# Kernel tuning notes

Hardware: AMD Instinct MI355X
Metric: run time of the kernel (lower is better)

Reference implementation:

```python
import jax, jax.numpy as jnp
import numpy as np

N = 100000          # n_nodes
E = 1600000         # n_edges (avg degree 16)
IN = 256            # in_dim
OUT = 16            # out_dim
SLOPE = 0.2         # leaky_relu negative slope
DROP = 0.5          # dropout rate


def _xavier(key, shape):
    fan_in, fan_out = shape
    std = (2.0 / (fan_in + fan_out)) ** 0.5
    return std * jax.random.normal(key, shape, jnp.float32)


def setup_inputs() -> dict:
    key = jax.random.key(0)
    ks = jax.random.split(key, 10)
    x = jax.random.normal(ks[0], (N, IN), jnp.float32)
    row = jax.random.randint(ks[1], (E,), 0, N, jnp.int32)
    col = jax.random.randint(ks[2], (E,), 0, N, jnp.int32)
    edge_w = jax.random.uniform(ks[3], (E,), jnp.float32)
    W1 = _xavier(ks[4], (IN, IN // 2)); b1 = jnp.zeros((IN // 2,), jnp.float32)
    W2 = _xavier(ks[5], (IN // 2, IN // 4)); b2 = jnp.zeros((IN // 4,), jnp.float32)
    W3 = _xavier(ks[6], (IN // 4, IN // 8)); b3 = jnp.zeros((IN // 8,), jnp.float32)
    W4 = _xavier(ks[7], (IN // 8, OUT)); b4 = jnp.zeros((OUT,), jnp.float32)
    # dropout mask (training-mode dropout made deterministic; pre-scaled by 1/(1-p))
    drop_mask = (jax.random.uniform(ks[8], (N, IN // 2)) > DROP).astype(jnp.float32) / (1.0 - DROP)
    return dict(x=x, row=row, col=col, edge_w=edge_w,
                W1=W1, b1=b1, W2=W2, b2=b2, W3=W3, b3=b3, W4=W4, b4=b4,
                drop_mask=drop_mask)


def reference(x, row, col, edge_w, W1, b1, W2, b2, W3, b3, W4, b4, drop_mask):
    def spmm(h):
        # out[i] = sum over edges (i <- j): w_ij * h[j]   (sparse adj @ h)
        return jax.ops.segment_sum(edge_w[:, None] * h[col], row, num_segments=N)

    lrelu = lambda v: jax.nn.leaky_relu(v, SLOPE)

    h = spmm(x @ W1) + b1          # gc1: [N, IN/2]
    h = lrelu(h) * drop_mask       # leaky_relu + dropout
    h = spmm(h @ W2) + b2          # gc2: [N, IN/4]
    h = lrelu(h)
    h = lrelu(h @ W3 + b3)         # clf hidden: [N, IN/8]
    return h @ W4 + b4             # logits: [N, OUT]
```

## Files before the change

kernel.cpp:

```cpp
#include <hip/hip_runtime.h>
#include <hip/hip_bf16.h>

#define N_NODES 100000
#define N_EDGES 1600000
#define SLOPE_ 0.2f
#define NBK 196
#define BCAP 9216
#define NCB 25
#define KEYS (512 * NCB)
#define BINBLK 256

typedef __attribute__((ext_vector_type(8))) short bf16x8;
typedef __attribute__((ext_vector_type(4))) float f32x4;

__device__ __forceinline__ short f2bf(float f) {
    __hip_bfloat16 h = __float2bfloat16(f);
    return *reinterpret_cast<short*>(&h);
}
__device__ __forceinline__ float bflo(unsigned u) { return __uint_as_float(u << 16); }
__device__ __forceinline__ float bfhi(unsigned u) { return __uint_as_float(u & 0xFFFF0000u); }
__device__ __forceinline__ float bf2f(short s) {
    return __uint_as_float(((unsigned)(unsigned short)s) << 16);
}


__global__ void passA_k(const int* __restrict__ row, const int* __restrict__ col,
                        const float* __restrict__ ew, int* __restrict__ cur,
                        int2* __restrict__ binned) {
    __shared__ int hist[NBK], base[NBK], off[NBK];
    int t = threadIdx.x;
    const int chunk = N_EDGES / BINBLK;
    int e0 = blockIdx.x * chunk;
    for (int i = t; i < NBK; i += 256) { hist[i] = 0; off[i] = 0; }
    __syncthreads();
    for (int i = t; i < chunk; i += 256) {
        int b = row[e0 + i] >> 9;
        atomicAdd(&hist[b], 1);
    }
    __syncthreads();
    for (int i = t; i < NBK; i += 256)
        base[i] = atomicAdd(&cur[i], hist[i]);
    __syncthreads();
    for (int i = t; i < chunk; i += 256) {
        int e = e0 + i;
        int r = row[e], c = col[e];
        int b = r >> 9;
        int p = base[b] + atomicAdd(&off[b], 1);
        if (p < BCAP)
            binned[(size_t)b * BCAP + p] =
                make_int2(((r & 511) << 17) | c, __float_as_int(ew[e]));
    }
}


__global__ void __launch_bounds__(512) passB_k(const int2* __restrict__ binned,
                                               const int* __restrict__ cur,
                                               int2* __restrict__ cw,
                                               int* __restrict__ row_ptr) {
    __shared__ int hist[KEYS];
    __shared__ int offs[KEYS];
    __shared__ int ssum[512];
    __shared__ int bexc[256];
    int t = threadIdx.x, b = blockIdx.x;
    const int2* src = binned + (size_t)b * BCAP;
    int cnt = cur[b];
    if (cnt > BCAP) cnt = BCAP;

    if (t < 256) bexc[t] = (t < NBK) ? min(cur[t], BCAP) : 0;
    __syncthreads();
    for (int off2 = 1; off2 < 256; off2 <<= 1) {
        int v = (t < 256 && t >= off2) ? bexc[t - off2] : 0;
        __syncthreads();
        if (t < 256) bexc[t] += v;
        __syncthreads();
    }
    int gbase = bexc[b] - cnt;

    for (int i = t; i < KEYS; i += 512) hist[i] = 0;
    __syncthreads();

    for (int i = t; i < cnt; i += 512) {
        int2 v = src[i];
        int c = v.x & 0x1FFFF, lr = v.x >> 17;
        atomicAdd(&hist[lr * NCB + (c >> 12)], 1);
    }
    __syncthreads();

    int loc[NCB];
    int tot = 0;
#pragma unroll
    for (int j = 0; j < NCB; j++) {
        loc[j] = tot;
        tot += hist[t * NCB + j];
    }
    ssum[t] = tot;
    __syncthreads();
    for (int off2 = 1; off2 < 512; off2 <<= 1) {
        int v = (t >= off2) ? ssum[t - off2] : 0;
        __syncthreads();
        ssum[t] += v;
        __syncthreads();
    }
    int base = ssum[t] - tot;
#pragma unroll
    for (int j = 0; j < NCB; j++) offs[t * NCB + j] = base + loc[j];

    int grow = b * 512 + t;
    if (grow <= N_NODES) row_ptr[grow] = gbase + base;
    __syncthreads();

    for (int i = t; i < cnt; i += 512) {
        int2 v = src[i];
        int c = v.x & 0x1FFFF, lr = v.x >> 17;
        int p = gbase + atomicAdd(&offs[lr * NCB + (c >> 12)], 1);
        cw[p] = make_int2(c, v.y);
    }
}


__global__ void prep_k(const float* __restrict__ W1, const float* __restrict__ W2,
                       short* __restrict__ Bp1, short* __restrict__ Bp2) {
    int i = blockIdx.x * 256 + threadIdx.x;
    if (i < 4096) {
        int ln = i & 15, nt = (i >> 4) & 7, g = (i >> 7) & 3, ks = i >> 9;
        int n = nt * 16 + ln, k0 = ks * 32 + g * 8;
        bf16x8 v;
#pragma unroll
        for (int j = 0; j < 8; j++) v[j] = f2bf(W1[(k0 + j) * 128 + n]);
        *(bf16x8*)(Bp1 + (size_t)i * 8) = v;
    } else if (i < 5120) {
        int c = i - 4096;
        int ln = c & 15, nt = (c >> 4) & 3, g = (c >> 6) & 3, ks = c >> 8;
        int n = nt * 16 + ln, k0 = ks * 32 + g * 8;
        bf16x8 v;
#pragma unroll
        for (int j = 0; j < 8; j++) v[j] = f2bf(W2[(k0 + j) * 64 + n]);
        *(bf16x8*)(Bp2 + (size_t)c * 8) = v;
    }
}


template <int K, int COLS, bool ABF16>
__global__ __launch_bounds__(512) void gemm_p(const void* __restrict__ Ap,
                                              const short* __restrict__ Bp,
                                              short* __restrict__ out, int M) {
    constexpr int NT = COLS / 16;
    constexpr int NKS = K / 32;
    __shared__ short Bs[K * COLS];
    int t = threadIdx.x;
    for (int i = t; i < K * COLS / 8; i += 512)
        *(bf16x8*)(Bs + (size_t)i * 8) = *(const bf16x8*)(Bp + (size_t)i * 8);
    __syncthreads();

    int l = t & 63, wv = t >> 6;
    int ln = l & 15, g = l >> 4;
    int row0 = blockIdx.x * 256 + wv * 32;
    int r0 = row0 + ln, r1 = row0 + 16 + ln;
    int cr0 = min(r0, M - 1), cr1 = min(r1, M - 1);

    f32x4 acc[2][NT];
#pragma unroll
    for (int rf = 0; rf < 2; rf++)
#pragma unroll
        for (int nt = 0; nt < NT; nt++) acc[rf][nt] = (f32x4){0.f, 0.f, 0.f, 0.f};

#pragma unroll
    for (int ks = 0; ks < NKS; ks++) {
        int kk = ks * 32 + g * 8;
        bf16x8 a0, a1;
        if constexpr (ABF16) {
            a0 = *(const bf16x8*)((const short*)Ap + (size_t)cr0 * K + kk);
            a1 = *(const bf16x8*)((const short*)Ap + (size_t)cr1 * K + kk);
        } else {
            const float* p0 = (const float*)Ap + (size_t)cr0 * K + kk;
            const float* p1 = (const float*)Ap + (size_t)cr1 * K + kk;
            float4 u0 = *(const float4*)p0;
            float4 u1 = *(const float4*)(p0 + 4);
            float4 v0 = *(const float4*)p1;
            float4 v1 = *(const float4*)(p1 + 4);
            a0[0] = f2bf(u0.x); a0[1] = f2bf(u0.y); a0[2] = f2bf(u0.z); a0[3] = f2bf(u0.w);
            a0[4] = f2bf(u1.x); a0[5] = f2bf(u1.y); a0[6] = f2bf(u1.z); a0[7] = f2bf(u1.w);
            a1[0] = f2bf(v0.x); a1[1] = f2bf(v0.y); a1[2] = f2bf(v0.z); a1[3] = f2bf(v0.w);
            a1[4] = f2bf(v1.x); a1[5] = f2bf(v1.y); a1[6] = f2bf(v1.z); a1[7] = f2bf(v1.w);
        }
#pragma unroll
        for (int nt = 0; nt < NT; nt++) {
            bf16x8 b = *(const bf16x8*)(Bs + (size_t)((((ks * 4 + g) * NT + nt) * 16 + ln)) * 8);
            acc[0][nt] = __builtin_amdgcn_mfma_f32_16x16x32_bf16(a0, b, acc[0][nt], 0, 0, 0);
            acc[1][nt] = __builtin_amdgcn_mfma_f32_16x16x32_bf16(a1, b, acc[1][nt], 0, 0, 0);
        }
    }
#pragma unroll
    for (int rf = 0; rf < 2; rf++)
#pragma unroll
        for (int nt = 0; nt < NT; nt++)
#pragma unroll
            for (int r = 0; r < 4; r++) {
                int orow = row0 + rf * 16 + g * 4 + r;
                if (orow < M) out[(size_t)orow * COLS + nt * 16 + ln] = f2bf(acc[rf][nt][r]);
            }
}


template <int D, bool DROP>
__global__ void spmm_bf(const int* __restrict__ row_ptr, const int2* __restrict__ cw,
                        const short* __restrict__ h,
                        const float* __restrict__ bias, const float* __restrict__ mask,
                        short* __restrict__ out, int n) {
    int bid = blockIdx.x;
    int sbid = (bid & 7) * 3125 + (bid >> 3);
    int wid = sbid * 4 + (int)(threadIdx.x >> 6);
    int lane = threadIdx.x & 63;
    if (wid >= n) return;
    int s = row_ptr[wid], e = row_ptr[wid + 1];
    float ax = 0.f, ay = 0.f;
    int base = s;
    while (base < e) {
        int m = e - base;
        if (m > 64) m = 64;
        int2 cwv = (lane < m) ? cw[base + lane] : make_int2(0, 0);
        int j = 0;
        for (; j + 4 <= m; j += 4) {
            int c0 = __shfl(cwv.x, j);     float w0 = __uint_as_float(__shfl(cwv.y, j));
            int c1 = __shfl(cwv.x, j + 1); float w1 = __uint_as_float(__shfl(cwv.y, j + 1));
            int c2 = __shfl(cwv.x, j + 2); float w2 = __uint_as_float(__shfl(cwv.y, j + 2));
            int c3 = __shfl(cwv.x, j + 3); float w3 = __uint_as_float(__shfl(cwv.y, j + 3));
            if (D == 128) {
                unsigned u0 = *(const unsigned*)(h + (size_t)c0 * 128 + 2 * lane);
                unsigned u1 = *(const unsigned*)(h + (size_t)c1 * 128 + 2 * lane);
                unsigned u2 = *(const unsigned*)(h + (size_t)c2 * 128 + 2 * lane);
                unsigned u3 = *(const unsigned*)(h + (size_t)c3 * 128 + 2 * lane);
                ax += w0 * bflo(u0); ay += w0 * bfhi(u0);
                ax += w1 * bflo(u1); ay += w1 * bfhi(u1);
                ax += w2 * bflo(u2); ay += w2 * bfhi(u2);
                ax += w3 * bflo(u3); ay += w3 * bfhi(u3);
            } else {
                float v0 = bf2f(h[(size_t)c0 * 64 + lane]);
                float v1 = bf2f(h[(size_t)c1 * 64 + lane]);
                float v2 = bf2f(h[(size_t)c2 * 64 + lane]);
                float v3 = bf2f(h[(size_t)c3 * 64 + lane]);
                ax += w0 * v0 + w1 * v1 + w2 * v2 + w3 * v3;
            }
        }
        for (; j < m; j++) {
            int c0 = __shfl(cwv.x, j);
            float w0 = __uint_as_float(__shfl(cwv.y, j));
            if (D == 128) {
                unsigned u0 = *(const unsigned*)(h + (size_t)c0 * 128 + 2 * lane);
                ax += w0 * bflo(u0); ay += w0 * bfhi(u0);
            } else {
                ax += w0 * bf2f(h[(size_t)c0 * 64 + lane]);
            }
        }
        base += m;
    }
    if (D == 128) {
        float2 b = *(const float2*)(bias + 2 * lane);
        float ox = ax + b.x, oy = ay + b.y;
        ox = ox > 0.f ? ox : SLOPE_ * ox;
        oy = oy > 0.f ? oy : SLOPE_ * oy;
        if (DROP) {
            float2 m2 = *(const float2*)(mask + (size_t)wid * 128 + 2 * lane);
            ox *= m2.x;
            oy *= m2.y;
        }
        unsigned ov = (unsigned)(unsigned short)f2bf(ox) |
                      ((unsigned)(unsigned short)f2bf(oy) << 16);
        *(unsigned*)(out + (size_t)wid * 128 + 2 * lane) = ov;
    } else {
        float o = ax + bias[lane];
        o = o > 0.f ? o : SLOPE_ * o;
        out[(size_t)wid * 64 + lane] = f2bf(o);
    }
}


__global__ void clf_k(const short* __restrict__ h, const float* __restrict__ W3,
                      const float* __restrict__ b3, const float* __restrict__ W4,
                      const float* __restrict__ b4, float* __restrict__ out) {
    __shared__ float W3s[64][32];
    __shared__ float W4s[32][16];
    __shared__ float b3s[32], b4s[16];
    __shared__ float hs[32][64];
    __shared__ float t4[32][33];
    int t = threadIdx.x;
    for (int l = t; l < 64 * 32; l += 256) W3s[l / 32][l % 32] = W3[l];
    for (int l = t; l < 32 * 16; l += 256) W4s[l / 16][l % 16] = W4[l];
    if (t < 32) b3s[t] = b3[t];
    if (t < 16) b4s[t] = b4[t];
    int row0 = blockIdx.x * 32;
    {
        bf16x8 v = *(const bf16x8*)(h + (size_t)row0 * 64 + t * 8);
        int r = t >> 3, c0 = (t & 7) << 3;
#pragma unroll
        for (int j = 0; j < 8; j++) hs[r][c0 + j] = bf2f(v[j]);
    }
    __syncthreads();
    for (int l = t; l < 1024; l += 256) {
        int r = l / 32, c = l % 32;
        float a = b3s[c];
#pragma unroll 8
        for (int k = 0; k < 64; k++) a += hs[r][k] * W3s[k][c];
        t4[r][c] = a > 0.f ? a : SLOPE_ * a;
    }
    __syncthreads();
    for (int l = t; l < 512; l += 256) {
        int r = l / 16, c = l % 16;
        float a = b4s[c];
#pragma unroll
        for (int k = 0; k < 32; k++) a += t4[r][k] * W4s[k][c];
        out[(size_t)(row0 + r) * 16 + c] = a;
    }
}


extern "C" void kernel_launch(void* const* d_in, const int* in_sizes, int n_in,
                              void* d_out, int out_size, void* d_ws, size_t ws_size,
                              hipStream_t stream) {
    const float* x = (const float*)d_in[0];
    const int* row = (const int*)d_in[1];
    const int* col = (const int*)d_in[2];
    const float* ew = (const float*)d_in[3];
    const float* W1 = (const float*)d_in[4];
    const float* b1 = (const float*)d_in[5];
    const float* W2 = (const float*)d_in[6];
    const float* b2 = (const float*)d_in[7];
    const float* W3 = (const float*)d_in[8];
    const float* b3 = (const float*)d_in[9];
    const float* W4 = (const float*)d_in[10];
    const float* b4 = (const float*)d_in[11];
    const float* mask = (const float*)d_in[12];
    float* out = (float*)d_out;

    const int N = N_NODES, E = N_EDGES;

    short* h0 = (short*)d_ws;
    short* h1 = h0 + (size_t)N * 128;
    short* h2 = h1 + (size_t)N * 128;
    short* h3 = h2 + (size_t)N * 64;
    short* Bp1 = h3 + (size_t)N * 64;
    short* Bp2 = Bp1 + 32768;
    int* row_ptr = (int*)(Bp2 + 8192);
    int* cur = row_ptr + N + 1;
    int2* cw = (int2*)(cur + NBK + 3);
    int2* binned = (int2*)h0;

    hipMemsetAsync(cur, 0, NBK * sizeof(int), stream);
    passA_k<<<BINBLK, 256, 0, stream>>>(row, col, ew, cur, binned);
    passB_k<<<NBK, 512, 0, stream>>>(binned, cur, cw, row_ptr);
    prep_k<<<20, 256, 0, stream>>>(W1, W2, Bp1, Bp2);

    gemm_p<256, 128, false><<<(N + 255) / 256, 512, 0, stream>>>(x, Bp1, h0, N);
    spmm_bf<128, true><<<25000, 256, 0, stream>>>(row_ptr, cw, h0, b1, mask, h1, N);
    gemm_p<128, 64, true><<<(N + 255) / 256, 512, 0, stream>>>(h1, Bp2, h2, N);
    spmm_bf<64, false><<<25000, 256, 0, stream>>>(row_ptr, cw, h2, b2, nullptr, h3, N);
    clf_k<<<N / 32, 256, 0, stream>>>(h3, W3, b3, W4, b4, out);
}
```

Measured before the change: 256.5 us.

## Pack dropout mask to bits, widen SpMM unroll, half-wave D=64 gather, coarser column bins

The float dropout mask is packed into a bitmask in a separate kernel, and the first SpMM reads bits and applies a hardcoded 2x scale. The SpMM inner loops are unrolled to 8 edges. In the D=64 variant each half-wave handles a different edge and the halves are combined with a shuffle. Edge loads and output stores use nontemporal hints, and the CSR column sub-bins are made coarser (13 instead of 25). The mask pass still reads the whole float mask every call, which adds a kernel and only pays off if the cheaper SpMM mask read outweighs it. The hardcoded 2.0 assumes the mask holds only 0 or 1/(1-p).

```diff
diff --git a/kernel.cpp b/kernel.cpp
--- a/kernel.cpp
+++ b/kernel.cpp
@@ -6,7 +6,7 @@
 #define SLOPE_ 0.2f
 #define NBK 196
 #define BCAP 9216
-#define NCB 25
+#define NCB 13
 #define KEYS (512 * NCB)
 #define BINBLK 256
 
@@ -82,7 +82,7 @@
     for (int i = t; i < cnt; i += 512) {
         int2 v = src[i];
         int c = v.x & 0x1FFFF, lr = v.x >> 17;
-        atomicAdd(&hist[lr * NCB + (c >> 12)], 1);
+        atomicAdd(&hist[lr * NCB + (c >> 13)], 1);
     }
     __syncthreads();
 
@@ -112,7 +112,7 @@
     for (int i = t; i < cnt; i += 512) {
         int2 v = src[i];
         int c = v.x & 0x1FFFF, lr = v.x >> 17;
-        int p = gbase + atomicAdd(&offs[lr * NCB + (c >> 12)], 1);
+        int p = gbase + atomicAdd(&offs[lr * NCB + (c >> 13)], 1);
         cw[p] = make_int2(c, v.y);
     }
 }
@@ -137,6 +137,23 @@
         for (int j = 0; j < 8; j++) v[j] = f2bf(W2[(k0 + j) * 64 + n]);
         *(bf16x8*)(Bp2 + (size_t)c * 8) = v;
     }
+}
+
+
+__global__ void packmask_k(const float* __restrict__ m, unsigned* __restrict__ mp) {
+    int i = blockIdx.x * 256 + threadIdx.x;
+    if (i >= N_NODES * 4) return;
+    const float4* p = (const float4*)(m + (size_t)i * 32);
+    unsigned b = 0;
+#pragma unroll
+    for (int j = 0; j < 8; j++) {
+        float4 v = p[j];
+        b |= (unsigned)(v.x != 0.f) << (4 * j);
+        b |= (unsigned)(v.y != 0.f) << (4 * j + 1);
+        b |= (unsigned)(v.z != 0.f) << (4 * j + 2);
+        b |= (unsigned)(v.w != 0.f) << (4 * j + 3);
+    }
+    mp[i] = b;
 }
 
 
@@ -205,7 +222,7 @@
 template <int D, bool DROP>
 __global__ void spmm_bf(const int* __restrict__ row_ptr, const int2* __restrict__ cw,
                         const short* __restrict__ h,
-                        const float* __restrict__ bias, const float* __restrict__ mask,
+                        const float* __restrict__ bias, const unsigned* __restrict__ maskp,
                         short* __restrict__ out, int n) {
     int bid = blockIdx.x;
     int sbid = (bid & 7) * 3125 + (bid >> 3);
@@ -218,38 +235,65 @@
     while (base < e) {
         int m = e - base;
         if (m > 64) m = 64;
-        int2 cwv = (lane < m) ? cw[base + lane] : make_int2(0, 0);
+        int2 cwv = make_int2(0, 0);
+        if (lane < m) {
+            unsigned long long cu =
+                __builtin_nontemporal_load((const unsigned long long*)(cw + base) + lane);
+            cwv.x = (int)(cu & 0xFFFFFFFFull);
+            cwv.y = (int)(cu >> 32);
+        }
         int j = 0;
-        for (; j + 4 <= m; j += 4) {
-            int c0 = __shfl(cwv.x, j);     float w0 = __uint_as_float(__shfl(cwv.y, j));
-            int c1 = __shfl(cwv.x, j + 1); float w1 = __uint_as_float(__shfl(cwv.y, j + 1));
-            int c2 = __shfl(cwv.x, j + 2); float w2 = __uint_as_float(__shfl(cwv.y, j + 2));
-            int c3 = __shfl(cwv.x, j + 3); float w3 = __uint_as_float(__shfl(cwv.y, j + 3));
-            if (D == 128) {
+        if (D == 128) {
+            for (; j + 8 <= m; j += 8) {
+                unsigned u[8];
+                float w[8];
+#pragma unroll
+                for (int p = 0; p < 8; p++) {
+                    int c = __shfl(cwv.x, j + p);
+                    w[p] = __uint_as_float(__shfl(cwv.y, j + p));
+                    u[p] = *(const unsigned*)(h + (size_t)c * 128 + 2 * lane);
+                }
+#pragma unroll
+                for (int p = 0; p < 8; p++) {
+                    ax += w[p] * bflo(u[p]);
+                    ay += w[p] * bfhi(u[p]);
+                }
+            }
+            for (; j < m; j++) {
+                int c0 = __shfl(cwv.x, j);
+                float w0 = __uint_as_float(__shfl(cwv.y, j));
                 unsigned u0 = *(const unsigned*)(h + (size_t)c0 * 128 + 2 * lane);
-                unsigned u1 = *(const unsigned*)(h + (size_t)c1 * 128 + 2 * lane);
-                unsigned u2 = *(const unsigned*)(h + (size_t)c2 * 128 + 2 * lane);
-                unsigned u3 = *(const unsigned*)(h + (size_t)c3 * 128 + 2 * lane);
-                ax += w0 * bflo(u0); ay += w0 * bfhi(u0);
-                ax += w1 * bflo(u1); ay += w1 * bfhi(u1);
-                ax += w2 * bflo(u2); ay += w2 * bfhi(u2);
-                ax += w3 * bflo(u3); ay += w3 * bfhi(u3);
-            } else {
-                float v0 = bf2f(h[(size_t)c0 * 64 + lane]);
-                float v1 = bf2f(h[(size_t)c1 * 64 + lane]);
-                float v2 = bf2f(h[(size_t)c2 * 64 + lane]);
-                float v3 = bf2f(h[(size_t)c3 * 64 + lane]);
-                ax += w0 * v0 + w1 * v1 + w2 * v2 + w3 * v3;
+                ax += w0 * bflo(u0);
+                ay += w0 * bfhi(u0);
             }
-        }
-        for (; j < m; j++) {
-            int c0 = __shfl(cwv.x, j);
-            float w0 = __uint_as_float(__shfl(cwv.y, j));
-            if (D == 128) {
-                unsigned u0 = *(const unsigned*)(h + (size_t)c0 * 128 + 2 * lane);
-                ax += w0 * bflo(u0); ay += w0 * bfhi(u0);
-            } else {
-                ax += w0 * bf2f(h[(size_t)c0 * 64 + lane]);
+        } else {
+            for (; j + 8 <= m; j += 8) {
+                unsigned u[4];
+                float w[4];
+#pragma unroll
+                for (int p = 0; p < 4; p++) {
+                    int eA = j + 2 * p, eB = eA + 1;
+                    int cA = __shfl(cwv.x, eA), cB = __shfl(cwv.x, eB);
+                    float wA = __uint_as_float(__shfl(cwv.y, eA));
+                    float wB = __uint_as_float(__shfl(cwv.y, eB));
+                    int myc = (lane < 32) ? cA : cB;
+                    w[p] = (lane < 32) ? wA : wB;
+                    u[p] = *(const unsigned*)(h + (size_t)myc * 64 + (lane & 31) * 2);
+                }
+#pragma unroll
+                for (int p = 0; p < 4; p++) {
+                    ax += w[p] * bflo(u[p]);
+                    ay += w[p] * bfhi(u[p]);
+                }
+            }
+            for (; j < m; j++) {
+                int c0 = __shfl(cwv.x, j);
+                float w0 = __uint_as_float(__shfl(cwv.y, j));
+                if (lane < 32) {
+                    unsigned u0 = *(const unsigned*)(h + (size_t)c0 * 64 + (lane & 31) * 2);
+                    ax += w0 * bflo(u0);
+                    ay += w0 * bfhi(u0);
+                }
             }
         }
         base += m;
@@ -260,17 +304,25 @@
         ox = ox > 0.f ? ox : SLOPE_ * ox;
         oy = oy > 0.f ? oy : SLOPE_ * oy;
         if (DROP) {
-            float2 m2 = *(const float2*)(mask + (size_t)wid * 128 + 2 * lane);
-            ox *= m2.x;
-            oy *= m2.y;
+            unsigned mw = maskp[(size_t)wid * 4 + (lane >> 4)];
+            unsigned sh = (2 * lane) & 31;
+            ox = ((mw >> sh) & 1u) ? 2.f * ox : 0.f;
+            oy = ((mw >> (sh + 1)) & 1u) ? 2.f * oy : 0.f;
         }
         unsigned ov = (unsigned)(unsigned short)f2bf(ox) |
                       ((unsigned)(unsigned short)f2bf(oy) << 16);
-        *(unsigned*)(out + (size_t)wid * 128 + 2 * lane) = ov;
+        __builtin_nontemporal_store(ov, (unsigned*)(out + (size_t)wid * 128 + 2 * lane));
     } else {
-        float o = ax + bias[lane];
-        o = o > 0.f ? o : SLOPE_ * o;
-        out[(size_t)wid * 64 + lane] = f2bf(o);
+        ax += __shfl_xor(ax, 32);
+        ay += __shfl_xor(ay, 32);
+        float2 b = *(const float2*)(bias + (lane & 31) * 2);
+        float ox = ax + b.x, oy = ay + b.y;
+        ox = ox > 0.f ? ox : SLOPE_ * ox;
+        oy = oy > 0.f ? oy : SLOPE_ * oy;
+        unsigned ov = (unsigned)(unsigned short)f2bf(ox) |
+                      ((unsigned)(unsigned short)f2bf(oy) << 16);
+        if (lane < 32)
+            __builtin_nontemporal_store(ov, (unsigned*)(out + (size_t)wid * 64 + lane * 2));
     }
 }
 
@@ -342,16 +394,18 @@
     short* Bp2 = Bp1 + 32768;
     int* row_ptr = (int*)(Bp2 + 8192);
     int* cur = row_ptr + N + 1;
-    int2* cw = (int2*)(cur + NBK + 3);
+    unsigned* mask_p = (unsigned*)(cur + NBK + 3);
+    int2* cw = (int2*)(mask_p + (size_t)N * 4);
     int2* binned = (int2*)h0;
 
     hipMemsetAsync(cur, 0, NBK * sizeof(int), stream);
     passA_k<<<BINBLK, 256, 0, stream>>>(row, col, ew, cur, binned);
     passB_k<<<NBK, 512, 0, stream>>>(binned, cur, cw, row_ptr);
     prep_k<<<20, 256, 0, stream>>>(W1, W2, Bp1, Bp2);
+    packmask_k<<<(N * 4 + 255) / 256, 256, 0, stream>>>(mask, mask_p);
 
     gemm_p<256, 128, false><<<(N + 255) / 256, 512, 0, stream>>>(x, Bp1, h0, N);
-    spmm_bf<128, true><<<25000, 256, 0, stream>>>(row_ptr, cw, h0, b1, mask, h1, N);
+    spmm_bf<128, true><<<25000, 256, 0, stream>>>(row_ptr, cw, h0, b1, mask_p, h1, N);
     gemm_p<128, 64, true><<<(N + 255) / 256, 512, 0, stream>>>(h1, Bp2, h2, N);
     spmm_bf<64, false><<<25000, 256, 0, stream>>>(row_ptr, cw, h2, b2, nullptr, h3, N);
     clf_k<<<N / 32, 256, 0, stream>>>(h3, W3, b3, W4, b4, out);
```

Measured after the change: 265.1 us. 3.3% more time.
